# Performance work log

Measured on AMD Instinct MI355X. Metric: run time of the kernel, lower is better.

## Reference

```python
import jax, jax.numpy as jnp
import numpy as np

LATENT = 100
INIT_SIZE = 8   # img_size // 4
NUM = 200       # LIF time steps
BETA = 0.95
THR = 1.0
CH_OUT = 3

# snntorch ATan surrogate spike (alpha=2 -> grad = 1/(1+(pi*u)^2))
@jax.custom_vjp
def spike_fn(x):
    return (x > 0).astype(x.dtype)

def _spike_fwd(x):
    return (x > 0).astype(x.dtype), x

def _spike_bwd(x, g):
    return (g / (1.0 + (jnp.pi * x) ** 2),)

spike_fn.defvjp(_spike_fwd, _spike_bwd)

def batchnorm(x, gamma, beta, eps):
    # training-mode BN: batch statistics over (N,H,W), biased variance (as torch)
    mean = x.mean(axis=(0, 2, 3), keepdims=True)
    var = ((x - mean) ** 2).mean(axis=(0, 2, 3), keepdims=True)
    xh = (x - mean) * jax.lax.rsqrt(var + eps)
    return xh * gamma[None, :, None, None] + beta[None, :, None, None]

def upsample2x(x):  # nearest-neighbor, scale 2
    return jnp.repeat(jnp.repeat(x, 2, axis=2), 2, axis=3)

def conv2d(x, w, b):  # 3x3, stride 1, padding 1
    y = jax.lax.conv_general_dilated(x, w, (1, 1), [(1, 1), (1, 1)],
                                     dimension_numbers=("NCHW", "OIHW", "NCHW"))
    return y + b[None, :, None, None]

def leaky_relu(x):
    return jnp.where(x >= 0, x, 0.2 * x)

def setup_inputs() -> dict:
    key = jax.random.key(0)
    ks = jax.random.split(key, 8)
    B = 8
    def n(k, shape, s=0.02):
        return jax.random.normal(k, shape, dtype=jnp.float32) * s
    return {
        "z": jax.random.normal(ks[0], (B, LATENT), dtype=jnp.float32),
        "w_l1": n(ks[1], (LATENT, 128 * INIT_SIZE ** 2)),
        "b_l1": jnp.zeros((128 * INIT_SIZE ** 2,), jnp.float32),
        "g1": jnp.ones((128,), jnp.float32), "be1": jnp.zeros((128,), jnp.float32),
        "w_c1": n(ks[2], (128, NUM * 128, 3, 3), 0.005),
        "b_c1": jnp.zeros((128,), jnp.float32),
        "g2": jnp.ones((128,), jnp.float32), "be2": jnp.zeros((128,), jnp.float32),
        "w_c2": n(ks[3], (64, 128, 3, 3)),
        "b_c2": jnp.zeros((64,), jnp.float32),
        "g3": jnp.ones((64,), jnp.float32), "be3": jnp.zeros((64,), jnp.float32),
        "w_c3": n(ks[4], (CH_OUT, 64, 3, 3)),
        "b_c3": jnp.zeros((CH_OUT,), jnp.float32),
    }

def reference(z, w_l1, b_l1, g1, be1, w_c1, b_c1, g2, be2, w_c2, b_c2, g3, be3, w_c3, b_c3):
    B = z.shape[0]
    out = z @ w_l1 + b_l1                       # (B, 128*8*8)
    out = out.reshape(B, 128, INIT_SIZE, INIT_SIZE)
    out = batchnorm(out, g1, be1, 1e-5)
    out = upsample2x(out)                       # (B,128,16,16) constant LIF input

    def lif_step(mem, _):
        # snntorch Leaky, reset-by-subtraction; reset detached from grad
        reset = jax.lax.stop_gradient((mem > THR).astype(mem.dtype))
        mem = BETA * mem + out - reset * THR
        spk = spike_fn(mem - THR)
        return mem, spk

    mem0 = jnp.zeros_like(out)
    _, spk_rec = jax.lax.scan(lif_step, mem0, None, length=NUM)  # (NUM,B,128,16,16)
    # faithful to torch.stack(dim=0).reshape(B, -1, 16, 16)
    x = spk_rec.reshape(B, NUM * 128, 16, 16)
    x = conv2d(x, w_c1, b_c1)                   # (B,128,16,16)
    x = leaky_relu(batchnorm(x, g2, be2, 0.8))  # BatchNorm2d(128, 0.8): eps=0.8
    x = upsample2x(x)                           # (B,128,32,32)
    x = conv2d(x, w_c2, b_c2)                   # (B,64,32,32)
    x = leaky_relu(batchnorm(x, g3, be3, 0.8))
    x = conv2d(x, w_c3, b_c3)                   # (B,3,32,32)
    return jnp.tanh(x)
```

## Files before the change

kernel.cpp:

```cpp
#include <hip/hip_runtime.h>
#include <math.h>


#define WROW 25632
#define SROW 25664

typedef _Float16 half8 __attribute__((ext_vector_type(8)));
typedef float f32x4 __attribute__((ext_vector_type(4)));
typedef unsigned int uint4v __attribute__((ext_vector_type(4)));

union AFrag { uint4v u4; unsigned int u[4]; half8 h; };

__global__ __launch_bounds__(256) void k_linear(
    const float* __restrict__ z, const float* __restrict__ w,
    const float* __restrict__ bias, float* __restrict__ out) {
  int g = blockIdx.x * 256 + threadIdx.x;
  int b = g >> 13, j = g & 8191;
  float acc = bias[j];
  const float* zp = z + b * 100;
  for (int l = 0; l < 100; ++l) acc += zp[l] * w[l * 8192 + j];
  out[g] = acc;
}

__global__ __launch_bounds__(256) void k_bn1_up(
    const float* __restrict__ lin, const float* __restrict__ g1,
    const float* __restrict__ be1, float* __restrict__ I) {
  int ch = blockIdx.x, tid = threadIdx.x;
  __shared__ float red[256];
  int n0 = tid, n1 = tid + 256;
  float v0 = lin[(n0 >> 6) * 8192 + ch * 64 + (n0 & 63)];
  float v1 = lin[(n1 >> 6) * 8192 + ch * 64 + (n1 & 63)];
  red[tid] = v0 + v1; __syncthreads();
  for (int s = 128; s > 0; s >>= 1) { if (tid < s) red[tid] += red[tid + s]; __syncthreads(); }
  float mean = red[0] * (1.0f / 512.0f);
  __syncthreads();
  float d0 = v0 - mean, d1 = v1 - mean;
  red[tid] = d0 * d0 + d1 * d1; __syncthreads();
  for (int s = 128; s > 0; s >>= 1) { if (tid < s) red[tid] += red[tid + s]; __syncthreads(); }
  float var = red[0] * (1.0f / 512.0f);
  float coef = g1[ch] / sqrtf(var + 1e-5f);
  float beta = be1[ch];
  float q0 = (v0 - mean) * coef + beta;
  float q1 = (v1 - mean) * coef + beta;
#pragma unroll
  for (int k = 0; k < 2; ++k) {
    int n = k ? n1 : n0; float q = k ? q1 : q0;
    int b = n >> 6, hw = n & 63, h = hw >> 3, w = hw & 7;
    float* o = I + (size_t)(b * 128 + ch) * 256 + (2 * h) * 16 + 2 * w;
    o[0] = q; o[1] = q; o[16] = q; o[17] = q;
  }
}

__global__ __launch_bounds__(256) void k_lif(
    const float* __restrict__ I, unsigned char* __restrict__ spkTb) {
  int g = blockIdx.x * 256 + threadIdx.x;
  int px = g >> 10, plane = g & 1023;
  int lane = threadIdx.x & 63;
  float in = I[plane * 256 + px];
  int pos = ((px >> 4) + 1) * 18 + (px & 15) + 1;
  unsigned long long* wsrow =
      (unsigned long long*)(spkTb + (size_t)pos * SROW + ((plane - lane) >> 3));
  float mem = 0.0f;
  for (int t = 0; t < 200; ++t) {
    float reset = (mem > 1.0f) ? 1.0f : 0.0f;
    mem = 0.95f * mem + in - reset;
    unsigned long long m = __ballot(mem > 1.0f);
    if (lane == 0) wsrow[t * 16] = m;
  }
}

__global__ __launch_bounds__(256) void k_wtrans(
    const float* __restrict__ wc1, _Float16* __restrict__ wT) {
  __shared__ float t[2304];
  int oc = blockIdx.x / 100, cg = blockIdx.x % 100;
  int c0 = cg * 256, tid = threadIdx.x;
  const float* src = wc1 + (size_t)oc * 230400 + (size_t)c0 * 9;
#pragma unroll
  for (int i = 0; i < 9; ++i) t[tid + i * 256] = src[tid + i * 256];
  __syncthreads();
#pragma unroll
  for (int tap = 0; tap < 9; ++tap)
    wT[(size_t)(tap * 128 + oc) * WROW + c0 + tid] = (_Float16)t[tid * 9 + tap];
}

__device__ inline void expandp(unsigned int b, AFrag& f) {
  unsigned int lo = ((b & 0xFu) * 0x00204081u) & 0x01010101u;
  unsigned int hi = ((b >> 4) * 0x00204081u) & 0x01010101u;
  lo *= 0x3Cu; hi *= 0x3Cu;
  f.u[0] = __builtin_amdgcn_perm(0u, lo, 0x01040004u);
  f.u[1] = __builtin_amdgcn_perm(0u, lo, 0x03040204u);
  f.u[2] = __builtin_amdgcn_perm(0u, hi, 0x01040004u);
  f.u[3] = __builtin_amdgcn_perm(0u, hi, 0x03040204u);
}

__device__ __forceinline__ void gll16(const void* g, void* l) {
  __builtin_amdgcn_global_load_lds(
      (const __attribute__((address_space(1))) unsigned int*)g,
      (__attribute__((address_space(3))) unsigned int*)l, 16, 0, 0);
}

__global__ __launch_bounds__(256, 3) void k_conv1_mfma(
    const unsigned char* __restrict__ spkTb, const _Float16* __restrict__ wT,
    _Float16* __restrict__ y1p) {
  int v = (blockIdx.x & 7) * 100 + (blockIdx.x >> 3);
  int tl = v >> 4, half = (v >> 3) & 1, b = v & 7;
  int tid = threadIdx.x;
  int wave = tid >> 6, lane = tid & 63;
  int quad = lane >> 4, l16 = lane & 15;
  int qs = quad * 8;
  int h0 = wave * 4;

  __shared__ _Float16 As[2][8192];

  const char* wb = (const char*)wT + (size_t)tl * 1024;
  const char* srcA[4];
#pragma unroll
  for (int i = 0; i < 4; ++i) {
    int oc = i * 16 + (tid >> 4);
    int sc = (tid & 15) ^ (oc & 7);
    srcA[i] = wb + (size_t)(half * 64 + oc) * (WROW * 2) + sc * 16;
  }

  const unsigned char* sb = spkTb + b * 3200 + tl * 64;

  int dsb[4];
#pragma unroll
  for (int s = 0; s < 4; ++s)
    dsb[s] = l16 * 256 + ((s * 64 + quad * 16) ^ ((l16 & 7) << 4));

  f32x4 acc[4][4] = {};
  uint4v bx[2][4];

#pragma unroll
  for (int i = 0; i < 4; ++i)
    gll16(srcA[i], (char*)As[0] + i * 4096 + wave * 1024);
#pragma unroll
  for (int nt = 0; nt < 4; ++nt) {
    int pos = (h0 + nt) * 18 + l16;
    bx[0][nt] = *(const uint4v*)(sb + (size_t)pos * SROW);
  }
  __syncthreads();

#pragma unroll 2
  for (int bs = 0; bs < 36; ++bs) {
    int cur = bs & 1;
    if (bs + 1 < 36) {
      int bn = bs + 1;
      int tap = bn >> 2, s128 = bn & 3;
      int dh = tap / 3, dw = tap - dh * 3;
#pragma unroll
      for (int nt = 0; nt < 4; ++nt) {
        int pos = (h0 + nt + dh) * 18 + l16 + dw;
        bx[bn & 1][nt] = *(const uint4v*)(sb + (size_t)pos * SROW + s128 * 16);
      }
      size_t aoff = (size_t)tap * ((size_t)128 * WROW * 2) + (size_t)s128 * 256;
#pragma unroll
      for (int i = 0; i < 4; ++i)
        gll16(srcA[i] + aoff, (char*)As[bn & 1] + i * 4096 + wave * 1024);
    }
    const char* cA = (const char*)As[cur];
#pragma unroll
    for (int s = 0; s < 4; ++s) {
      AFrag a[4];
#pragma unroll
      for (int mt = 0; mt < 4; ++mt)
        a[mt].u4 = *(const uint4v*)(cA + dsb[s] + mt * 4096);
#pragma unroll
      for (int nt = 0; nt < 4; ++nt) {
        AFrag bf; expandp((bx[cur][nt][s] >> qs) & 0xFFu, bf);
#pragma unroll
        for (int mt = 0; mt < 4; ++mt)
          acc[mt][nt] = __builtin_amdgcn_mfma_f32_16x16x32_f16(
              a[mt].h, bf.h, acc[mt][nt], 0, 0, 0);
      }
    }
    __syncthreads();
  }

  _Float16* ob = y1p + (size_t)(tl * 8 + b) * 32768 + half * 16384;
#pragma unroll
  for (int mt = 0; mt < 4; ++mt)
#pragma unroll
    for (int nt = 0; nt < 4; ++nt) {
      int px = wave * 64 + nt * 16 + l16;
#pragma unroll
      for (int r = 0; r < 4; ++r) {
        int oc = mt * 16 + quad * 4 + r;
        ob[(size_t)oc * 256 + px] = (_Float16)acc[mt][nt][r];
      }
    }
}

__global__ __launch_bounds__(256) void k_reduce1(
    const _Float16* __restrict__ y1p, float* __restrict__ y1) {
  int g = (blockIdx.x * 256 + threadIdx.x) * 2;
  const char* p = (const char*)y1p + (size_t)g * 2;
  float a0 = 0.0f, a1 = 0.0f;
#pragma unroll 5
  for (int tl = 0; tl < 50; ++tl) {
    union { unsigned int u; _Float16 h[2]; } cv;
    cv.u = *(const unsigned int*)(p + (size_t)tl * 524288);
    a0 += (float)cv.h[0];
    a1 += (float)cv.h[1];
  }
  y1[g] = a0; y1[g + 1] = a1;
}

__global__ __launch_bounds__(256) void k_bn2_up(
    const float* __restrict__ y1, const float* __restrict__ bc1,
    const float* __restrict__ g2, const float* __restrict__ be2,
    float* __restrict__ x2p) {
  int ch = blockIdx.x, tid = threadIdx.x;
  __shared__ float red[256];
  float bias = bc1[ch];
  float v[8]; float s = 0.0f;
#pragma unroll
  for (int k = 0; k < 8; ++k) {
    int n = tid + k * 256;
    v[k] = y1[(size_t)((n >> 8) * 128 + ch) * 256 + (n & 255)] + bias;
    s += v[k];
  }
  red[tid] = s; __syncthreads();
  for (int st = 128; st > 0; st >>= 1) { if (tid < st) red[tid] += red[tid + st]; __syncthreads(); }
  float mean = red[0] * (1.0f / 2048.0f);
  __syncthreads();
  s = 0.0f;
#pragma unroll
  for (int k = 0; k < 8; ++k) { float d = v[k] - mean; s += d * d; }
  red[tid] = s; __syncthreads();
  for (int st = 128; st > 0; st >>= 1) { if (tid < st) red[tid] += red[tid + st]; __syncthreads(); }
  float var = red[0] * (1.0f / 2048.0f);
  float coef = g2[ch] / sqrtf(var + 0.8f);
  float beta = be2[ch];
#pragma unroll
  for (int k = 0; k < 8; ++k) {
    int n = tid + k * 256;
    int b = n >> 8, px = n & 255, h = px >> 4, w = px & 15;
    float q = (v[k] - mean) * coef + beta;
    q = (q >= 0.0f) ? q : 0.2f * q;
    float* o = x2p + (size_t)(b * 128 + ch) * 1156 + (2 * h + 1) * 34 + (2 * w + 1);
    o[0] = q; o[1] = q; o[34] = q; o[35] = q;
  }
}

__global__ __launch_bounds__(256) void k_conv2(
    const float* __restrict__ x2p, const float* __restrict__ wc2,
    const float* __restrict__ bc2, float* __restrict__ y2) {
  int octile = blockIdx.x, b = blockIdx.y, tid = threadIdx.x;
  float acc[16];
#pragma unroll
  for (int i = 0; i < 16; ++i) acc[i] = 0.0f;
  const float* base = x2p + (size_t)(b * 128) * 1156;
  for (int ch = 0; ch < 128; ++ch) {
    const float* pl = base + (size_t)ch * 1156;
    float sv[4][9];
#pragma unroll
    for (int j = 0; j < 4; ++j) {
      int p = tid + j * 256, h = p >> 5, w = p & 31;
      const float* pp = pl + h * 34 + w;
      sv[j][0] = pp[0];  sv[j][1] = pp[1];  sv[j][2] = pp[2];
      sv[j][3] = pp[34]; sv[j][4] = pp[35]; sv[j][5] = pp[36];
      sv[j][6] = pp[68]; sv[j][7] = pp[69]; sv[j][8] = pp[70];
    }
#pragma unroll
    for (int ol = 0; ol < 4; ++ol) {
      const float* wp = wc2 + (size_t)((octile * 4 + ol) * 128 + ch) * 9;
#pragma unroll
      for (int j = 0; j < 4; ++j) {
        acc[ol * 4 + j] += sv[j][0] * wp[0] + sv[j][1] * wp[1] + sv[j][2] * wp[2]
                         + sv[j][3] * wp[3] + sv[j][4] * wp[4] + sv[j][5] * wp[5]
                         + sv[j][6] * wp[6] + sv[j][7] * wp[7] + sv[j][8] * wp[8];
      }
    }
  }
#pragma unroll
  for (int ol = 0; ol < 4; ++ol) {
    int oc = octile * 4 + ol;
    float bias = bc2[oc];
#pragma unroll
    for (int j = 0; j < 4; ++j)
      y2[(size_t)(b * 64 + oc) * 1024 + tid + j * 256] = acc[ol * 4 + j] + bias;
  }
}

__global__ __launch_bounds__(256) void k_bn3(
    const float* __restrict__ y2, const float* __restrict__ g3,
    const float* __restrict__ be3, float* __restrict__ y2n) {
  int ch = blockIdx.x, tid = threadIdx.x;
  __shared__ float red[256];
  float v[32]; float s = 0.0f;
#pragma unroll
  for (int k = 0; k < 32; ++k) {
    int n = tid + k * 256;
    v[k] = y2[(size_t)((n >> 10) * 64 + ch) * 1024 + (n & 1023)];
    s += v[k];
  }
  red[tid] = s; __syncthreads();
  for (int st = 128; st > 0; st >>= 1) { if (tid < st) red[tid] += red[tid + st]; __syncthreads(); }
  float mean = red[0] * (1.0f / 8192.0f);
  __syncthreads();
  s = 0.0f;
#pragma unroll
  for (int k = 0; k < 32; ++k) { float d = v[k] - mean; s += d * d; }
  red[tid] = s; __syncthreads();
  for (int st = 128; st > 0; st >>= 1) { if (tid < st) red[tid] += red[tid + st]; __syncthreads(); }
  float var = red[0] * (1.0f / 8192.0f);
  float coef = g3[ch] / sqrtf(var + 0.8f);
  float beta = be3[ch];
#pragma unroll
  for (int k = 0; k < 32; ++k) {
    int n = tid + k * 256;
    int b = n >> 10, px = n & 1023, h = px >> 5, w = px & 31;
    float q = (v[k] - mean) * coef + beta;
    q = (q >= 0.0f) ? q : 0.2f * q;
    y2n[(size_t)(b * 64 + ch) * 1156 + (h + 1) * 34 + (w + 1)] = q;
  }
}

__global__ __launch_bounds__(256) void k_conv3(
    const float* __restrict__ y2n, const float* __restrict__ wc3,
    const float* __restrict__ bc3, float* __restrict__ out) {
  int quarter = blockIdx.x & 3, b = blockIdx.x >> 2;
  int p = quarter * 256 + threadIdx.x, h = p >> 5, w = p & 31;
  float a0 = 0.0f, a1 = 0.0f, a2 = 0.0f;
  const float* base = y2n + (size_t)(b * 64) * 1156 + h * 34 + w;
  for (int ch = 0; ch < 64; ++ch) {
    const float* pp = base + (size_t)ch * 1156;
    float s0 = pp[0],  s1 = pp[1],  s2 = pp[2];
    float s3 = pp[34], s4 = pp[35], s5 = pp[36];
    float s6 = pp[68], s7 = pp[69], s8 = pp[70];
    const float* w0 = wc3 + (size_t)ch * 9;
    const float* w1 = wc3 + (size_t)(64 + ch) * 9;
    const float* w2 = wc3 + (size_t)(128 + ch) * 9;
    a0 += s0*w0[0]+s1*w0[1]+s2*w0[2]+s3*w0[3]+s4*w0[4]+s5*w0[5]+s6*w0[6]+s7*w0[7]+s8*w0[8];
    a1 += s0*w1[0]+s1*w1[1]+s2*w1[2]+s3*w1[3]+s4*w1[4]+s5*w1[5]+s6*w1[6]+s7*w1[7]+s8*w1[8];
    a2 += s0*w2[0]+s1*w2[1]+s2*w2[2]+s3*w2[3]+s4*w2[4]+s5*w2[5]+s6*w2[6]+s7*w2[7]+s8*w2[8];
  }
  out[(size_t)(b * 3 + 0) * 1024 + p] = tanhf(a0 + bc3[0]);
  out[(size_t)(b * 3 + 1) * 1024 + p] = tanhf(a1 + bc3[1]);
  out[(size_t)(b * 3 + 2) * 1024 + p] = tanhf(a2 + bc3[2]);
}

extern "C" void kernel_launch(void* const* d_in, const int* in_sizes, int n_in,
                              void* d_out, int out_size, void* d_ws, size_t ws_size,
                              hipStream_t stream) {
  const float* z    = (const float*)d_in[0];
  const float* w_l1 = (const float*)d_in[1];
  const float* b_l1 = (const float*)d_in[2];
  const float* g1   = (const float*)d_in[3];
  const float* be1  = (const float*)d_in[4];
  const float* w_c1 = (const float*)d_in[5];
  const float* b_c1 = (const float*)d_in[6];
  const float* g2   = (const float*)d_in[7];
  const float* be2  = (const float*)d_in[8];
  const float* w_c2 = (const float*)d_in[9];
  const float* b_c2 = (const float*)d_in[10];
  const float* g3   = (const float*)d_in[11];
  const float* be3  = (const float*)d_in[12];
  const float* w_c3 = (const float*)d_in[13];
  const float* b_c3 = (const float*)d_in[14];
  float* out = (float*)d_out;

  char* ws = (char*)d_ws;
  _Float16* wT = (_Float16*)ws;
  unsigned char* spkTb = (unsigned char*)(ws + 59056128);
  float* lin = (float*)(ws + 67371264);
  float* I   = (float*)(ws + 67633408);
  float* y1  = (float*)(ws + 68681984);
  _Float16* y1p = (_Float16*)(ws + 69730560);
  float* x2p = (float*)ws;
  float* y2n = (float*)(ws + 4734976);
  float* y2  = (float*)(ws + 7102464);

  size_t spkTb_bytes = (size_t)324 * SROW;

  hipMemsetAsync(spkTb, 0, spkTb_bytes, stream);

  k_wtrans <<<12800, 256, 0, stream>>>(w_c1, wT);
  k_linear <<<256, 256, 0, stream>>>(z, w_l1, b_l1, lin);
  k_bn1_up <<<128, 256, 0, stream>>>(lin, g1, be1, I);
  k_lif    <<<1024, 256, 0, stream>>>(I, spkTb);
  k_conv1_mfma<<<800, 256, 0, stream>>>(spkTb, wT, y1p);
  k_reduce1<<<512, 256, 0, stream>>>(y1p, y1);

  hipMemsetAsync(x2p, 0, (size_t)1183744 * 4, stream);
  hipMemsetAsync(y2n, 0, (size_t)591872 * 4, stream);

  k_bn2_up <<<128, 256, 0, stream>>>(y1, b_c1, g2, be2, x2p);
  k_conv2  <<<dim3(16, 8), 256, 0, stream>>>(x2p, w_c2, b_c2, y2);
  k_bn3    <<<64, 256, 0, stream>>>(y2, g3, be3, y2n);
  k_conv3  <<<32, 256, 0, stream>>>(y2n, w_c3, b_c3, out);
}
```

Baseline: 524.5 us.

## Triple-buffer conv1 weight tiles with explicit vmcnt waits and raw barriers

The conv1 MFMA kernel now keeps three LDS weight buffers and prefetches two k-steps ahead instead of one. It replaces __syncthreads with manual s_waitcnt vmcnt counts plus s_barrier, and raises wave priority around the MFMA block. The loop is unrolled by 6 so buffer indices are compile-time constants. The goal is to hide global-to-LDS load latency behind more compute. The cost is 48KB of LDS per block, which may limit the three blocks per CU requested by the launch bounds, and the hand-counted vmcnt values must match the actual outstanding loads.

After: 523.0 us. Within noise of the previous version (-0.3%).

```diff
diff --git a/kernel.cpp b/kernel.cpp
--- a/kernel.cpp
+++ b/kernel.cpp
@@ -110,18 +110,14 @@
   int qs = quad * 8;
   int h0 = wave * 4;
 
-  __shared__ _Float16 As[2][8192];
+  __shared__ _Float16 As[3][8192];
 
   const char* wb = (const char*)wT + (size_t)tl * 1024;
-  const char* srcA[4];
-#pragma unroll
-  for (int i = 0; i < 4; ++i) {
-    int oc = i * 16 + (tid >> 4);
-    int sc = (tid & 15) ^ (oc & 7);
-    srcA[i] = wb + (size_t)(half * 64 + oc) * (WROW * 2) + sc * 16;
-  }
-
-  const unsigned char* sb = spkTb + b * 3200 + tl * 64;
+  int oc0 = (tid >> 4);
+  int sc0 = (tid & 15) ^ (oc0 & 7);
+  const char* srcA0 = wb + (size_t)(half * 64 + oc0) * (WROW * 2) + sc0 * 16;
+
+  const unsigned char* sbp = spkTb + b * 3200 + tl * 64;
 
   int dsb[4];
 #pragma unroll
@@ -132,49 +128,67 @@
   uint4v bx[2][4];
 
 #pragma unroll
-  for (int i = 0; i < 4; ++i)
-    gll16(srcA[i], (char*)As[0] + i * 4096 + wave * 1024);
-#pragma unroll
   for (int nt = 0; nt < 4; ++nt) {
     int pos = (h0 + nt) * 18 + l16;
-    bx[0][nt] = *(const uint4v*)(sb + (size_t)pos * SROW);
-  }
-  __syncthreads();
-
-#pragma unroll 2
-  for (int bs = 0; bs < 36; ++bs) {
-    int cur = bs & 1;
-    if (bs + 1 < 36) {
-      int bn = bs + 1;
-      int tap = bn >> 2, s128 = bn & 3;
-      int dh = tap / 3, dw = tap - dh * 3;
-#pragma unroll
-      for (int nt = 0; nt < 4; ++nt) {
-        int pos = (h0 + nt + dh) * 18 + l16 + dw;
-        bx[bn & 1][nt] = *(const uint4v*)(sb + (size_t)pos * SROW + s128 * 16);
+    bx[0][nt] = *(const uint4v*)(sbp + (size_t)pos * SROW);
+  }
+#pragma unroll
+  for (int i = 0; i < 4; ++i)
+    gll16(srcA0 + (size_t)i * (16 * WROW * 2), (char*)As + i * 4096 + wave * 1024);
+#pragma unroll
+  for (int i = 0; i < 4; ++i)
+    gll16(srcA0 + (size_t)i * (16 * WROW * 2) + 256,
+          (char*)As + 16384 + i * 4096 + wave * 1024);
+
+  for (int big = 0; big < 36; big += 6) {
+#pragma unroll
+    for (int u = 0; u < 6; ++u) {
+      int k = big + u;
+      if (k + 1 < 36) {
+        int j = k + 1;
+        int tap = j >> 2, s128 = j & 3;
+        int dh = tap / 3, dw = tap - dh * 3;
+#pragma unroll
+        for (int nt = 0; nt < 4; ++nt) {
+          int pos = (h0 + nt + dh) * 18 + l16 + dw;
+          bx[(u + 1) & 1][nt] =
+              *(const uint4v*)(sbp + (size_t)pos * SROW + s128 * 16);
+        }
       }
-      size_t aoff = (size_t)tap * ((size_t)128 * WROW * 2) + (size_t)s128 * 256;
-#pragma unroll
-      for (int i = 0; i < 4; ++i)
-        gll16(srcA[i] + aoff, (char*)As[bn & 1] + i * 4096 + wave * 1024);
+      if (k + 2 < 36) {
+        int j = k + 2;
+        int tap = j >> 2, s128 = j & 3;
+        size_t aoff = (size_t)tap * ((size_t)128 * WROW * 2) + (size_t)s128 * 256;
+        char* dst = (char*)As + ((u + 2) % 3) * 16384 + wave * 1024;
+#pragma unroll
+        for (int i = 0; i < 4; ++i)
+          gll16(srcA0 + (size_t)i * (16 * WROW * 2) + aoff, dst + i * 4096);
+      }
+      if (k + 2 < 36)      asm volatile("s_waitcnt vmcnt(8)" ::: "memory");
+      else if (k + 1 < 36) asm volatile("s_waitcnt vmcnt(4)" ::: "memory");
+      else                 asm volatile("s_waitcnt vmcnt(0)" ::: "memory");
+      __builtin_amdgcn_s_barrier();
+
+      const char* cA = (const char*)As + (u % 3) * 16384;
+      __builtin_amdgcn_s_setprio(1);
+#pragma unroll
+      for (int s = 0; s < 4; ++s) {
+        AFrag a[4];
+#pragma unroll
+        for (int mt = 0; mt < 4; ++mt)
+          a[mt].u4 = *(const uint4v*)(cA + dsb[s] + mt * 4096);
+#pragma unroll
+        for (int nt = 0; nt < 4; ++nt) {
+          AFrag bf; expandp((bx[u & 1][nt][s] >> qs) & 0xFFu, bf);
+#pragma unroll
+          for (int mt = 0; mt < 4; ++mt)
+            acc[mt][nt] = __builtin_amdgcn_mfma_f32_16x16x32_f16(
+                a[mt].h, bf.h, acc[mt][nt], 0, 0, 0);
+        }
+      }
+      __builtin_amdgcn_s_setprio(0);
+      __builtin_amdgcn_s_barrier();
     }
-    const char* cA = (const char*)As[cur];
-#pragma unroll
-    for (int s = 0; s < 4; ++s) {
-      AFrag a[4];
-#pragma unroll
-      for (int mt = 0; mt < 4; ++mt)
-        a[mt].u4 = *(const uint4v*)(cA + dsb[s] + mt * 4096);
-#pragma unroll
-      for (int nt = 0; nt < 4; ++nt) {
-        AFrag bf; expandp((bx[cur][nt][s] >> qs) & 0xFFu, bf);
-#pragma unroll
-        for (int mt = 0; mt < 4; ++mt)
-          acc[mt][nt] = __builtin_amdgcn_mfma_f32_16x16x32_f16(
-              a[mt].h, bf.h, acc[mt][nt], 0, 0, 0);
-      }
-    }
-    __syncthreads();
   }
 
   _Float16* ob = y1p + (size_t)(tl * 8 + b) * 32768 + half * 16384;
```

## Widen conv1 tile to two batches, fuse split-K reduce into BN2, drop memsets

Applied to the files above, without the earlier changes.

Each conv1 block now handles two batch images, so every staged weight tile in LDS feeds twice as many MFMAs. The grid halves to 400 blocks and occupancy drops to 2 blocks per CU. The spike B-fragments are now loaded synchronously each step instead of being double-buffered. The separate split-K reduce kernel is folded into the BN2 kernel, which sums the 50 fp16 partials itself, and the padded-buffer memsets are replaced by border zeroing inside the BN kernels. This trades fewer launches and less weight traffic for more registers per thread, possible load-latency stalls, and lower parallelism in the reduction.

Result: slower. 537.3 us (+2.4%).

```diff
diff --git a/kernel.cpp b/kernel.cpp
--- a/kernel.cpp
+++ b/kernel.cpp
@@ -99,11 +99,14 @@
       (__attribute__((address_space(3))) unsigned int*)l, 16, 0, 0);
 }
 
-__global__ __launch_bounds__(256, 3) void k_conv1_mfma(
+__global__ __launch_bounds__(256, 2) void k_conv1_mfma(
     const unsigned char* __restrict__ spkTb, const _Float16* __restrict__ wT,
     _Float16* __restrict__ y1p) {
-  int v = (blockIdx.x & 7) * 100 + (blockIdx.x >> 3);
-  int tl = v >> 4, half = (v >> 3) & 1, b = v & 7;
+  int v = (blockIdx.x & 7) * 50 + (blockIdx.x >> 3);
+  int tl = v >> 3;
+  int r = v & 7;
+  int half = r >> 2, bp = r & 3;
+  int b0 = bp * 2;
   int tid = threadIdx.x;
   int wave = tid >> 6, lane = tid & 63;
   int quad = lane >> 4, l16 = lane & 15;
@@ -112,53 +115,47 @@
 
   __shared__ _Float16 As[2][8192];
 
-  const char* wb = (const char*)wT + (size_t)tl * 1024;
-  const char* srcA[4];
-#pragma unroll
-  for (int i = 0; i < 4; ++i) {
-    int oc = i * 16 + (tid >> 4);
-    int sc = (tid & 15) ^ (oc & 7);
-    srcA[i] = wb + (size_t)(half * 64 + oc) * (WROW * 2) + sc * 16;
-  }
-
-  const unsigned char* sb = spkTb + b * 3200 + tl * 64;
+  int ocl = tid >> 4;
+  int sc0 = (tid & 15) ^ ocl;
+  const char* srcA0 = (const char*)wT + (size_t)tl * 1024
+                    + (size_t)(half * 64 + ocl) * (WROW * 2) + sc0 * 16;
+
+  const unsigned char* rowp[8];
+#pragma unroll
+  for (int nt = 0; nt < 8; ++nt)
+    rowp[nt] = spkTb + (b0 + (nt >> 2)) * 3200 + tl * 64
+             + (size_t)((h0 + (nt & 3)) * 18 + l16) * SROW;
 
   int dsb[4];
 #pragma unroll
   for (int s = 0; s < 4; ++s)
-    dsb[s] = l16 * 256 + ((s * 64 + quad * 16) ^ ((l16 & 7) << 4));
-
-  f32x4 acc[4][4] = {};
-  uint4v bx[2][4];
+    dsb[s] = l16 * 256 + ((s * 64 + quad * 16) ^ (l16 << 4));
+
+  f32x4 acc[4][8] = {};
 
 #pragma unroll
   for (int i = 0; i < 4; ++i)
-    gll16(srcA[i], (char*)As[0] + i * 4096 + wave * 1024);
-#pragma unroll
-  for (int nt = 0; nt < 4; ++nt) {
-    int pos = (h0 + nt) * 18 + l16;
-    bx[0][nt] = *(const uint4v*)(sb + (size_t)pos * SROW);
-  }
+    gll16(srcA0 + (size_t)i * (16 * WROW * 2), (char*)As + i * 4096 + wave * 1024);
   __syncthreads();
 
 #pragma unroll 2
   for (int bs = 0; bs < 36; ++bs) {
-    int cur = bs & 1;
+    int tap = bs >> 2, s128 = bs & 3;
+    int dh = tap / 3, dw = tap - dh * 3;
+    uint4v bx[8];
+    int boff = (dh * 18 + dw) * SROW + s128 * 16;
+#pragma unroll
+    for (int nt = 0; nt < 8; ++nt)
+      bx[nt] = *(const uint4v*)(rowp[nt] + boff);
     if (bs + 1 < 36) {
-      int bn = bs + 1;
-      int tap = bn >> 2, s128 = bn & 3;
-      int dh = tap / 3, dw = tap - dh * 3;
-#pragma unroll
-      for (int nt = 0; nt < 4; ++nt) {
-        int pos = (h0 + nt + dh) * 18 + l16 + dw;
-        bx[bn & 1][nt] = *(const uint4v*)(sb + (size_t)pos * SROW + s128 * 16);
-      }
-      size_t aoff = (size_t)tap * ((size_t)128 * WROW * 2) + (size_t)s128 * 256;
+      int tapn = (bs + 1) >> 2, s128n = (bs + 1) & 3;
+      size_t aoff = (size_t)tapn * ((size_t)128 * WROW * 2) + (size_t)s128n * 256;
+      char* dst = (char*)As + ((bs + 1) & 1) * 16384 + wave * 1024;
 #pragma unroll
       for (int i = 0; i < 4; ++i)
-        gll16(srcA[i] + aoff, (char*)As[bn & 1] + i * 4096 + wave * 1024);
-    }
-    const char* cA = (const char*)As[cur];
+        gll16(srcA0 + (size_t)i * (16 * WROW * 2) + aoff, dst + i * 4096);
+    }
+    const char* cA = (const char*)As + (bs & 1) * 16384;
 #pragma unroll
     for (int s = 0; s < 4; ++s) {
       AFrag a[4];
@@ -166,8 +163,8 @@
       for (int mt = 0; mt < 4; ++mt)
         a[mt].u4 = *(const uint4v*)(cA + dsb[s] + mt * 4096);
 #pragma unroll
-      for (int nt = 0; nt < 4; ++nt) {
-        AFrag bf; expandp((bx[cur][nt][s] >> qs) & 0xFFu, bf);
+      for (int nt = 0; nt < 8; ++nt) {
+        AFrag bf; expandp((bx[nt][s] >> qs) & 0xFFu, bf);
 #pragma unroll
         for (int mt = 0; mt < 4; ++mt)
           acc[mt][nt] = __builtin_amdgcn_mfma_f32_16x16x32_f16(
@@ -177,49 +174,52 @@
     __syncthreads();
   }
 
-  _Float16* ob = y1p + (size_t)(tl * 8 + b) * 32768 + half * 16384;
 #pragma unroll
   for (int mt = 0; mt < 4; ++mt)
 #pragma unroll
-    for (int nt = 0; nt < 4; ++nt) {
-      int px = wave * 64 + nt * 16 + l16;
-#pragma unroll
-      for (int r = 0; r < 4; ++r) {
-        int oc = mt * 16 + quad * 4 + r;
-        ob[(size_t)oc * 256 + px] = (_Float16)acc[mt][nt][r];
+    for (int nt = 0; nt < 8; ++nt) {
+      int bb = nt >> 2;
+      int px = (h0 + (nt & 3)) * 16 + l16;
+      _Float16* ob = y1p + (size_t)(tl * 8 + b0 + bb) * 32768 + half * 16384;
+#pragma unroll
+      for (int rr = 0; rr < 4; ++rr) {
+        int oc = mt * 16 + quad * 4 + rr;
+        ob[(size_t)oc * 256 + px] = (_Float16)acc[mt][nt][rr];
       }
     }
 }
 
-__global__ __launch_bounds__(256) void k_reduce1(
-    const _Float16* __restrict__ y1p, float* __restrict__ y1) {
-  int g = (blockIdx.x * 256 + threadIdx.x) * 2;
-  const char* p = (const char*)y1p + (size_t)g * 2;
-  float a0 = 0.0f, a1 = 0.0f;
-#pragma unroll 5
-  for (int tl = 0; tl < 50; ++tl) {
-    union { unsigned int u; _Float16 h[2]; } cv;
-    cv.u = *(const unsigned int*)(p + (size_t)tl * 524288);
-    a0 += (float)cv.h[0];
-    a1 += (float)cv.h[1];
-  }
-  y1[g] = a0; y1[g + 1] = a1;
-}
-
 __global__ __launch_bounds__(256) void k_bn2_up(
-    const float* __restrict__ y1, const float* __restrict__ bc1,
+    const _Float16* __restrict__ y1p, const float* __restrict__ bc1,
     const float* __restrict__ g2, const float* __restrict__ be2,
     float* __restrict__ x2p) {
   int ch = blockIdx.x, tid = threadIdx.x;
   __shared__ float red[256];
+
+  for (int e = tid; e < 1056; e += 256) {
+    int b = e / 132, i = e - b * 132;
+    int rr, cc;
+    if (i < 34)       { rr = 0;       cc = i; }
+    else if (i < 68)  { rr = 33;      cc = i - 34; }
+    else if (i < 100) { rr = i - 67;  cc = 0; }
+    else              { rr = i - 99;  cc = 33; }
+    x2p[(size_t)(b * 128 + ch) * 1156 + rr * 34 + cc] = 0.0f;
+  }
+
   float bias = bc1[ch];
+  float a[8];
+#pragma unroll
+  for (int k = 0; k < 8; ++k) a[k] = 0.0f;
+  const _Float16* base = y1p + (size_t)ch * 256 + tid;
+  for (int tl = 0; tl < 50; ++tl) {
+    const _Float16* p = base + (size_t)tl * 262144;
+#pragma unroll
+    for (int k = 0; k < 8; ++k) a[k] += (float)p[(size_t)k * 32768];
+  }
   float v[8]; float s = 0.0f;
 #pragma unroll
-  for (int k = 0; k < 8; ++k) {
-    int n = tid + k * 256;
-    v[k] = y1[(size_t)((n >> 8) * 128 + ch) * 256 + (n & 255)] + bias;
-    s += v[k];
-  }
+  for (int k = 0; k < 8; ++k) { v[k] = a[k] + bias; s += v[k]; }
+
   red[tid] = s; __syncthreads();
   for (int st = 128; st > 0; st >>= 1) { if (tid < st) red[tid] += red[tid + st]; __syncthreads(); }
   float mean = red[0] * (1.0f / 2048.0f);
@@ -234,8 +234,7 @@
   float beta = be2[ch];
 #pragma unroll
   for (int k = 0; k < 8; ++k) {
-    int n = tid + k * 256;
-    int b = n >> 8, px = n & 255, h = px >> 4, w = px & 15;
+    int b = k, px = tid, h = px >> 4, w = px & 15;
     float q = (v[k] - mean) * coef + beta;
     q = (q >= 0.0f) ? q : 0.2f * q;
     float* o = x2p + (size_t)(b * 128 + ch) * 1156 + (2 * h + 1) * 34 + (2 * w + 1);
@@ -288,6 +287,17 @@
     const float* __restrict__ be3, float* __restrict__ y2n) {
   int ch = blockIdx.x, tid = threadIdx.x;
   __shared__ float red[256];
+
+  for (int e = tid; e < 1056; e += 256) {
+    int b = e / 132, i = e - b * 132;
+    int rr, cc;
+    if (i < 34)       { rr = 0;       cc = i; }
+    else if (i < 68)  { rr = 33;      cc = i - 34; }
+    else if (i < 100) { rr = i - 67;  cc = 0; }
+    else              { rr = i - 99;  cc = 33; }
+    y2n[(size_t)(b * 64 + ch) * 1156 + rr * 34 + cc] = 0.0f;
+  }
+
   float v[32]; float s = 0.0f;
 #pragma unroll
   for (int k = 0; k < 32; ++k) {
@@ -366,7 +376,6 @@
   unsigned char* spkTb = (unsigned char*)(ws + 59056128);
   float* lin = (float*)(ws + 67371264);
   float* I   = (float*)(ws + 67633408);
-  float* y1  = (float*)(ws + 68681984);
   _Float16* y1p = (_Float16*)(ws + 69730560);
   float* x2p = (float*)ws;
   float* y2n = (float*)(ws + 4734976);
@@ -380,13 +389,9 @@
   k_linear <<<256, 256, 0, stream>>>(z, w_l1, b_l1, lin);
   k_bn1_up <<<128, 256, 0, stream>>>(lin, g1, be1, I);
   k_lif    <<<1024, 256, 0, stream>>>(I, spkTb);
-  k_conv1_mfma<<<800, 256, 0, stream>>>(spkTb, wT, y1p);
-  k_reduce1<<<512, 256, 0, stream>>>(y1p, y1);
-
-  hipMemsetAsync(x2p, 0, (size_t)1183744 * 4, stream);
-  hipMemsetAsync(y2n, 0, (size_t)591872 * 4, stream);
-
-  k_bn2_up <<<128, 256, 0, stream>>>(y1, b_c1, g2, be2, x2p);
+  k_conv1_mfma<<<400, 256, 0, stream>>>(spkTb, wT, y1p);
+
+  k_bn2_up <<<128, 256, 0, stream>>>(y1p, b_c1, g2, be2, x2p);
   k_conv2  <<<dim3(16, 8), 256, 0, stream>>>(x2p, w_c2, b_c2, y2);
   k_bn3    <<<64, 256, 0, stream>>>(y2, g3, be3, y2n);
   k_conv3  <<<32, 256, 0, stream>>>(y2n, w_c3, b_c3, out);
```
